# Kernel optimization log

Measured on AMD Instinct MI355X. Metric: run time of the kernel, lower is better.

The kernel has to match this reference:

```python
import jax, jax.numpy as jnp
import numpy as np

TEMP = 1.0  # routing_temperature

def _gelu(x):
    return jax.nn.gelu(x, approximate=False)  # torch nn.GELU default (erf)

def setup_inputs() -> dict:
    key = jax.random.key(0)
    ks = jax.random.split(key, 6)
    B, S, D, E, I = 8, 2048, 768, 8, 3072
    H = I // 2
    def xav(k, shape):
        fan_in, fan_out = shape[-2], shape[-1]
        lim = float(np.sqrt(6.0 / (fan_in + fan_out)))
        return jax.random.uniform(k, shape, jnp.float32, -lim, lim)
    return {
        "x":  jax.random.normal(ks[0], (B, S, D), jnp.float32),
        "Wr": xav(ks[1], (D, E)),
        "br": jnp.zeros((E,), jnp.float32),
        "W1": xav(ks[2], (E, D, I)), "b1": jnp.zeros((E, I), jnp.float32),
        "W2": xav(ks[3], (E, I, H)), "b2": jnp.zeros((E, H), jnp.float32),
        "W3": xav(ks[4], (E, H, D)), "b3": jnp.zeros((E, D), jnp.float32),
        "top_k": 2,
    }

def reference(x, Wr, br, W1, b1, W2, b2, W3, b3, top_k):
    B, S, D = x.shape
    E = Wr.shape[1]
    T = B * S
    xt = x.reshape(T, D)                              # flatten tokens
    logits = (xt @ Wr + br) / TEMP                    # [T, E]
    vals, sel = jax.lax.top_k(logits, top_k)          # [T, k]
    w = jax.nn.softmax(vals, axis=-1)                 # softmax over top-k scores
    # dense per-token combine weights (zero for unselected experts)
    combine = jnp.zeros((T, E), x.dtype).at[jnp.arange(T)[:, None], sel].add(w)
    def step(acc, p):
        W1e, b1e, W2e, b2e, W3e, b3e, ce = p
        h = _gelu(xt @ W1e + b1e)                     # [T, I]
        h = _gelu(h @ W2e + b2e)                      # [T, I//2]
        y = h @ W3e + b3e                             # [T, D]
        return acc + ce[:, None] * y, None
    acc0 = jnp.zeros((T, D), x.dtype)
    out, _ = jax.lax.scan(step, acc0, (W1, b1, W2, b2, W3, b3, combine.T))
    return out.reshape(B, S, D)
```

## Files before the change

kernel.cpp:

```cpp
#include <hip/hip_runtime.h>
#include <hip/hip_fp16.h>
#include <cstdint>
#include <cstddef>

#define TK 16384
#define DD 768
#define EE 8
#define II 3072
#define HH 1536

typedef _Float16 half8 __attribute__((ext_vector_type(8)));
typedef float floatx4 __attribute__((ext_vector_type(4)));

typedef const __attribute__((address_space(1))) uint32_t* gptr_t;
typedef __attribute__((address_space(3))) uint32_t* lptr_t;

#define GLOAD_LDS16(gp, lp) __builtin_amdgcn_global_load_lds( \
    (gptr_t)(const void*)(gp), (lptr_t)(void*)(lp), 16, 0, 0)

__device__ __forceinline__ void xcd_swizzle(int& e, int& m, int& n, bool rev) {
  int gx = gridDim.x, gy = gridDim.y;
  int f = (blockIdx.z * gy + blockIdx.y) * gx + blockIdx.x;
  if (rev) f = gx * gy * 8 - 1 - f;
  int xcd = f & 7, idx = f >> 3;
  int chunk = idx / gx, pos = idx - chunk * gx;
  int logical = chunk * (8 * gx) + xcd * gx + pos;
  int mn = gy * gx;
  e = logical / mn;
  int rem = logical - e * mn;
  m = rem / gx;
  n = rem - m * gx;
}

__global__ __launch_bounds__(256)
void cvtT_kernel(const float* __restrict__ in, __half* __restrict__ out,
                 int K, int N) {
  __shared__ float tile[64][65];
  int e = blockIdx.z;
  const float* inp = in + (size_t)e * K * N + (size_t)(blockIdx.y * 64) * N + blockIdx.x * 64;
  __half* outp = out + (size_t)e * K * N + (size_t)(blockIdx.x * 64) * K + blockIdx.y * 64;
  int s = threadIdx.x;
  int tx = s & 15, r0 = s >> 4;
#pragma unroll
  for (int i = 0; i < 4; ++i) {
    int k = r0 + i * 16;
    float4 v = *(const float4*)&inp[(size_t)k * N + tx * 4];
    tile[k][tx * 4 + 0] = v.x;
    tile[k][tx * 4 + 1] = v.y;
    tile[k][tx * 4 + 2] = v.z;
    tile[k][tx * 4 + 3] = v.w;
  }
  __syncthreads();
  int kp = s & 31;
#pragma unroll
  for (int i = 0; i < 8; ++i) {
    int n = (s >> 5) + i * 8;
    __half2 h = __floats2half2_rn(tile[2 * kp][n], tile[2 * kp + 1][n]);
    *(__half2*)&outp[(size_t)n * K + kp * 2] = h;
  }
}

__global__ __launch_bounds__(256)
void router_kernel(const float* __restrict__ x, const float* __restrict__ Wr,
                   const float* __restrict__ br, int* __restrict__ counts,
                   int* __restrict__ sel, float* __restrict__ wTok,
                   __half* __restrict__ xh) {
  __shared__ float wr_s[EE * DD];
  for (int i = threadIdx.x; i < EE * DD; i += 256) {
    int d = i >> 3, e = i & 7;
    wr_s[e * DD + d] = Wr[i];
  }
  __syncthreads();
  int wid = threadIdx.x >> 6, lane = threadIdx.x & 63;
  int t = blockIdx.x * 4 + wid;
  const float* xt = x + (size_t)t * DD;
  float acc[EE];
#pragma unroll
  for (int e = 0; e < EE; ++e) acc[e] = 0.f;
  for (int d = lane; d < DD; d += 64) {
    float xv = xt[d];
#pragma unroll
    for (int e = 0; e < EE; ++e) acc[e] += xv * wr_s[e * DD + d];
  }
#pragma unroll
  for (int off = 32; off > 0; off >>= 1)
#pragma unroll
    for (int e = 0; e < EE; ++e) acc[e] += __shfl_xor(acc[e], off);
  if (lane == 0) {
    float v[EE];
#pragma unroll
    for (int e = 0; e < EE; ++e) v[e] = acc[e] + br[e];
    int i0 = 0;
#pragma unroll
    for (int e = 1; e < EE; ++e) if (v[e] > v[i0]) i0 = e;
    int i1 = (i0 == 0) ? 1 : 0;
#pragma unroll
    for (int e = 0; e < EE; ++e) if (e != i0 && v[e] > v[i1] && e != i1) { if (v[e] > v[i1]) i1 = e; }
    float e1 = __expf(v[i1] - v[i0]);
    float s = 1.f / (1.f + e1);
    sel[2 * t] = i0; sel[2 * t + 1] = i1;
    wTok[2 * t] = s; wTok[2 * t + 1] = e1 * s;
    atomicAdd(&counts[i0], 1);
    atomicAdd(&counts[i1], 1);
  }
  const float4* xr = (const float4*)xt;
  uint2* xo = (uint2*)(xh + (size_t)t * DD);
#pragma unroll
  for (int j = 0; j < 3; ++j) {
    float4 v = xr[lane + j * 64];
    __half2 a = __floats2half2_rn(v.x, v.y);
    __half2 b = __floats2half2_rn(v.z, v.w);
    uint2 p;
    p.x = *(const unsigned int*)&a;
    p.y = *(const unsigned int*)&b;
    xo[lane + j * 64] = p;
  }
}

__global__ void offsets_kernel(const int* __restrict__ counts, int* __restrict__ offsets,
                               int* __restrict__ cursors) {
  if (threadIdx.x == 0) {
    int o = 0;
    for (int e = 0; e < EE; ++e) { offsets[e] = o; cursors[e] = o; o += counts[e]; }
  }
}

__global__ void scatter_kernel(const int* __restrict__ sel, int* __restrict__ cursors,
                               int* __restrict__ idxList, int* __restrict__ posTok) {
  int t = blockIdx.x * 256 + threadIdx.x;
  if (t < TK) {
#pragma unroll
    for (int k = 0; k < 2; ++k) {
      int e = sel[2 * t + k];
      int p = atomicAdd(&cursors[e], 1);
      idxList[p] = t;
      posTok[2 * t + k] = p;
    }
  }
}

template<int KD, int ND, bool GATHER, bool GELU, bool REV>
__device__ __forceinline__
void ffn_body_big(const __half* __restrict__ A, const __half* __restrict__ Wt,
                  const float* __restrict__ Bias, __half* __restrict__ Out,
                  const int* __restrict__ counts, const int* __restrict__ offsets,
                  const int* __restrict__ idxList) {
  constexpr int NT = KD / 32;
  int e, mblk, nblk;
  xcd_swizzle(e, mblk, nblk, REV);
  const int cnt = counts[e];
  const int m0 = mblk * 256;
  if (cnt == 0 || m0 >= cnt) return;
  const int off = offsets[e];
  const int n0 = nblk * 256;
  const __half* We = Wt + (size_t)e * KD * ND;
  const float* be = Bias + (size_t)e * ND;

  __shared__ __align__(16) __half AsF[5 * 256 * 32];
  __shared__ __align__(16) __half BsF[4 * 256 * 32];

  const int tid = threadIdx.x;
  const int colh = (((tid & 3) ^ ((tid >> 3) & 3)) << 3);
  const __half* aptr2[2];
  const __half* bptr2[2];
#pragma unroll
  for (int i = 0; i < 2; ++i) {
    int r = i * 128 + (tid >> 2);
    int gr = m0 + r; if (gr > cnt - 1) gr = cnt - 1;
    size_t arow = GATHER ? (size_t)idxList[off + gr] : (size_t)(off + gr);
    aptr2[i] = A + arow * KD + colh;
    bptr2[i] = We + (size_t)(n0 + r) * KD + colh;
  }

#define STA(WOFF, TS) do { \
    GLOAD_LDS16(aptr2[0] + (TS) * 32, (char*)AsF + (WOFF) + tid * 16); \
    GLOAD_LDS16(aptr2[1] + (TS) * 32, (char*)AsF + (WOFF) + tid * 16 + 8192); } while (0)
#define STB(WOFF, TS) do { \
    GLOAD_LDS16(bptr2[0] + (TS) * 32, (char*)BsF + (WOFF) + tid * 16); \
    GLOAD_LDS16(bptr2[1] + (TS) * 32, (char*)BsF + (WOFF) + tid * 16 + 8192); } while (0)

  const int lane = tid & 63, wv = tid >> 6;
  const int wr = wv >> 2, wc = wv & 3;
  const int lrow = lane & 15, lg = lane >> 4;
  const int slotSwz = lg ^ ((lrow >> 1) & 3);
  const int aBase = (wr * 128 + lrow) * 64 + slotSwz * 16;
  const int bBase = (wc * 64 + lrow) * 64 + slotSwz * 16;

  floatx4 acc[8][4];
#pragma unroll
  for (int mi = 0; mi < 8; ++mi)
#pragma unroll
    for (int ni = 0; ni < 4; ++ni) acc[mi][ni] = (floatx4){0.f, 0.f, 0.f, 0.f};

  STA(0 * 16384, 0);
  STB(0 * 16384, 0);
  STA(1 * 16384, 1);
  STB(1 * 16384, 1);
  STA(2 * 16384, 2);
  STB(2 * 16384, 2);
  STA(3 * 16384, 3);
  asm volatile("s_waitcnt vmcnt(10)" ::: "memory");
  __builtin_amdgcn_s_barrier();
  __builtin_amdgcn_sched_barrier(0);

  int rA = 0, wA = 4 * 16384;
  int rB = 0, wB = 3 * 16384;

#pragma unroll 1
  for (int t = 0; t < NT; ++t) {
    half8 af[8], bf[4];
#pragma unroll
    for (int mi = 0; mi < 8; ++mi)
      af[mi] = *(const half8*)((const char*)AsF + rA + aBase + mi * 1024);
#pragma unroll
    for (int ni = 0; ni < 4; ++ni)
      bf[ni] = *(const half8*)((const char*)BsF + rB + bBase + ni * 1024);
    if (t + 3 < NT) STB(wB, t + 3);
    if (t + 4 < NT) STA(wA, t + 4);
    __builtin_amdgcn_s_setprio(1);
#pragma unroll
    for (int mi = 0; mi < 8; ++mi)
#pragma unroll
      for (int ni = 0; ni < 4; ++ni)
        acc[mi][ni] = __builtin_amdgcn_mfma_f32_16x16x32_f16(
            af[mi], bf[ni], acc[mi][ni], 0, 0, 0);
    __builtin_amdgcn_s_setprio(0);
    if (t + 4 < NT) { asm volatile("s_waitcnt vmcnt(10)" ::: "memory"); }
    else            { asm volatile("s_waitcnt vmcnt(0)"  ::: "memory"); }
    __builtin_amdgcn_s_barrier();
    __builtin_amdgcn_sched_barrier(0);
    rA += 16384; if (rA == 5 * 16384) rA = 0;
    wA += 16384; if (wA == 5 * 16384) wA = 0;
    rB += 16384; if (rB == 4 * 16384) rB = 0;
    wB += 16384; if (wB == 4 * 16384) wB = 0;
  }

  const int crow = m0 + wr * 128 + lg * 4;
  const int ccol = n0 + wc * 64 + lrow;
  float bv[4];
#pragma unroll
  for (int ni = 0; ni < 4; ++ni) bv[ni] = be[ccol + ni * 16];
#pragma unroll
  for (int mi = 0; mi < 8; ++mi) {
#pragma unroll
    for (int j = 0; j < 4; ++j) {
      int r = crow + mi * 16 + j;
      if (r < cnt) {
#pragma unroll
        for (int ni = 0; ni < 4; ++ni) {
          float v = acc[mi][ni][j] + bv[ni];
          if (GELU) v = 0.5f * v * (1.f + erff(v * 0.70710678118654752f));
          Out[(size_t)(off + r) * ND + ccol + ni * 16] = __float2half(v);
        }
      }
    }
  }
#undef STA
#undef STB
}

template<int KD, int ND, bool GATHER, bool GELU, bool REV>
__device__ __forceinline__
void ffn_body_small(const __half* __restrict__ A, const __half* __restrict__ Wt,
                    const float* __restrict__ Bias, __half* __restrict__ Out,
                    const int* __restrict__ counts, const int* __restrict__ offsets,
                    const int* __restrict__ idxList) {
  constexpr int NT = KD / 32;
  int e, mblk, nblk;
  xcd_swizzle(e, mblk, nblk, REV);
  const int cnt = counts[e];
  const int m0 = mblk * 128;
  if (cnt == 0 || m0 >= cnt) return;
  const int off = offsets[e];
  const int n0 = nblk * 128;
  const __half* We = Wt + (size_t)e * KD * ND;
  const float* be = Bias + (size_t)e * ND;

  __shared__ __align__(16) __half AsF[3 * 128 * 32];
  __shared__ __align__(16) __half BsF[3 * 128 * 32];

  const int tid = threadIdx.x;
  const int colh = (((tid & 3) ^ ((tid >> 3) & 3)) << 3);
  const __half* aptr2[2];
  const __half* bptr2[2];
#pragma unroll
  for (int i = 0; i < 2; ++i) {
    int r = i * 64 + (tid >> 2);
    int gr = m0 + r; if (gr > cnt - 1) gr = cnt - 1;
    size_t arow = GATHER ? (size_t)idxList[off + gr] : (size_t)(off + gr);
    aptr2[i] = A + arow * KD + colh;
    bptr2[i] = We + (size_t)(n0 + r) * KD + colh;
  }

#define STA(WOFF, TS) do { \
    GLOAD_LDS16(aptr2[0] + (TS) * 32, (char*)AsF + (WOFF) + tid * 16); \
    GLOAD_LDS16(aptr2[1] + (TS) * 32, (char*)AsF + (WOFF) + tid * 16 + 4096); } while (0)
#define STB(WOFF, TS) do { \
    GLOAD_LDS16(bptr2[0] + (TS) * 32, (char*)BsF + (WOFF) + tid * 16); \
    GLOAD_LDS16(bptr2[1] + (TS) * 32, (char*)BsF + (WOFF) + tid * 16 + 4096); } while (0)

  const int lane = tid & 63, wv = tid >> 6;
  const int wr = wv >> 1, wc = wv & 1;
  const int lrow = lane & 15, lg = lane >> 4;
  const int slotSwz = lg ^ ((lrow >> 1) & 3);
  const int aBase = (wr * 64 + lrow) * 64 + slotSwz * 16;
  const int bBase = (wc * 64 + lrow) * 64 + slotSwz * 16;

  floatx4 acc[4][4];
#pragma unroll
  for (int mi = 0; mi < 4; ++mi)
#pragma unroll
    for (int ni = 0; ni < 4; ++ni) acc[mi][ni] = (floatx4){0.f, 0.f, 0.f, 0.f};

  STB(0, 0);
  STA(0, 0);
  STB(8192, 1);
  STA(8192, 1);
  asm volatile("s_waitcnt vmcnt(4)" ::: "memory");
  __builtin_amdgcn_s_barrier();
  __builtin_amdgcn_sched_barrier(0);

  int rBuf = 0, wBuf = 2 * 8192;

#pragma unroll 1
  for (int t = 0; t < NT; ++t) {
    half8 af[4], bf[4];
#pragma unroll
    for (int mi = 0; mi < 4; ++mi)
      af[mi] = *(const half8*)((const char*)AsF + rBuf + aBase + mi * 1024);
#pragma unroll
    for (int ni = 0; ni < 4; ++ni)
      bf[ni] = *(const half8*)((const char*)BsF + rBuf + bBase + ni * 1024);
    if (t + 2 < NT) { STB(wBuf, t + 2); STA(wBuf, t + 2); }
    __builtin_amdgcn_s_setprio(1);
#pragma unroll
    for (int mi = 0; mi < 4; ++mi)
#pragma unroll
      for (int ni = 0; ni < 4; ++ni)
        acc[mi][ni] = __builtin_amdgcn_mfma_f32_16x16x32_f16(
            af[mi], bf[ni], acc[mi][ni], 0, 0, 0);
    __builtin_amdgcn_s_setprio(0);
    if (t + 2 < NT) { asm volatile("s_waitcnt vmcnt(4)" ::: "memory"); }
    else            { asm volatile("s_waitcnt vmcnt(0)" ::: "memory"); }
    __builtin_amdgcn_s_barrier();
    __builtin_amdgcn_sched_barrier(0);
    rBuf += 8192; if (rBuf == 3 * 8192) rBuf = 0;
    wBuf += 8192; if (wBuf == 3 * 8192) wBuf = 0;
  }

  const int crow = m0 + wr * 64 + lg * 4;
  const int ccol = n0 + wc * 64 + lrow;
  float bv[4];
#pragma unroll
  for (int ni = 0; ni < 4; ++ni) bv[ni] = be[ccol + ni * 16];
#pragma unroll
  for (int mi = 0; mi < 4; ++mi) {
#pragma unroll
    for (int j = 0; j < 4; ++j) {
      int r = crow + mi * 16 + j;
      if (r < cnt) {
#pragma unroll
        for (int ni = 0; ni < 4; ++ni) {
          float v = acc[mi][ni][j] + bv[ni];
          if (GELU) v = 0.5f * v * (1.f + erff(v * 0.70710678118654752f));
          Out[(size_t)(off + r) * ND + ccol + ni * 16] = __float2half(v);
        }
      }
    }
  }
#undef STA
#undef STB
}

__global__ __launch_bounds__(256, 2)
void ffn_s1(const __half* __restrict__ A, const __half* __restrict__ Wt,
            const float* __restrict__ Bias, __half* __restrict__ Out,
            const int* __restrict__ counts, const int* __restrict__ offsets,
            const int* __restrict__ idxL) {
  ffn_body_small<DD, II, true, true, false>(A, Wt, Bias, Out, counts, offsets, idxL);
}
__global__ __launch_bounds__(512, 1)
void ffn_s2(const __half* __restrict__ A, const __half* __restrict__ Wt,
            const float* __restrict__ Bias, __half* __restrict__ Out,
            const int* __restrict__ counts, const int* __restrict__ offsets,
            const int* __restrict__ idxL) {
  ffn_body_big<II, HH, false, true, true>(A, Wt, Bias, Out, counts, offsets, idxL);
}
__global__ __launch_bounds__(256, 2)
void ffn_s3(const __half* __restrict__ A, const __half* __restrict__ Wt,
            const float* __restrict__ Bias, __half* __restrict__ Out,
            const int* __restrict__ counts, const int* __restrict__ offsets,
            const int* __restrict__ idxL) {
  ffn_body_small<HH, DD, false, false, false>(A, Wt, Bias, Out, counts, offsets, idxL);
}

__global__ void combine_kernel(const __half* __restrict__ yc, const float* __restrict__ wTok,
                               const int* __restrict__ posTok, float* __restrict__ out) {
  int t = blockIdx.x;
  int d = threadIdx.x * 4;
  if (d >= DD) return;
  float w0 = wTok[2 * t], w1 = wTok[2 * t + 1];
  const __half2* a = (const __half2*)(yc + (size_t)posTok[2 * t] * DD + d);
  const __half2* b = (const __half2*)(yc + (size_t)posTok[2 * t + 1] * DD + d);
  float2 a0 = __half22float2(a[0]), a1 = __half22float2(a[1]);
  float2 b0 = __half22float2(b[0]), b1 = __half22float2(b[1]);
  float4 r;
  r.x = w0 * a0.x + w1 * b0.x;
  r.y = w0 * a0.y + w1 * b0.y;
  r.z = w0 * a1.x + w1 * b1.x;
  r.w = w0 * a1.y + w1 * b1.y;
  *(float4*)(out + (size_t)t * DD + d) = r;
}

extern "C" void kernel_launch(void* const* d_in, const int* in_sizes, int n_in,
                              void* d_out, int out_size, void* d_ws, size_t ws_size,
                              hipStream_t stream) {
  const float* x  = (const float*)d_in[0];
  const float* Wr = (const float*)d_in[1];
  const float* br = (const float*)d_in[2];
  const float* W1 = (const float*)d_in[3];
  const float* b1 = (const float*)d_in[4];
  const float* W2 = (const float*)d_in[5];
  const float* b2 = (const float*)d_in[6];
  const float* W3 = (const float*)d_in[7];
  const float* b3 = (const float*)d_in[8];
  float* out = (float*)d_out;

  char* ws = (char*)d_ws;
  size_t o = 0;
  auto alloc = [&](size_t bytes) {
    char* p = ws + o;
    o += (bytes + 255) & ~(size_t)255;
    return p;
  };
  __half* xh   = (__half*)alloc((size_t)TK * DD * 2);
  __half* w1t  = (__half*)alloc((size_t)EE * DD * II * 2);
  __half* w2t  = (__half*)alloc((size_t)EE * II * HH * 2);
  __half* w3t  = (__half*)alloc((size_t)EE * HH * DD * 2);
  __half* h1   = (__half*)alloc((size_t)2 * TK * II * 2);
  __half* h2   = (__half*)alloc((size_t)2 * TK * HH * 2);
  __half* yc   = (__half*)alloc((size_t)2 * TK * DD * 2);
  int*   idxL  = (int*)alloc(2 * TK * 4);
  int*   sel   = (int*)alloc(2 * TK * 4);
  float* wTok  = (float*)alloc(2 * TK * 4);
  int*   posT  = (int*)alloc(2 * TK * 4);
  int*   counts  = (int*)alloc(256);
  int*   offsets = (int*)alloc(256);
  int*   cursors = (int*)alloc(256);
  if (o > ws_size) return;

  hipMemsetAsync(counts, 0, 256, stream);

  cvtT_kernel<<<dim3(II / 64, DD / 64, EE), 256, 0, stream>>>(W1, w1t, DD, II);
  cvtT_kernel<<<dim3(HH / 64, II / 64, EE), 256, 0, stream>>>(W2, w2t, II, HH);
  cvtT_kernel<<<dim3(DD / 64, HH / 64, EE), 256, 0, stream>>>(W3, w3t, HH, DD);
  router_kernel<<<TK / 4, 256, 0, stream>>>(x, Wr, br, counts, sel, wTok, xh);
  offsets_kernel<<<1, 64, 0, stream>>>(counts, offsets, cursors);
  scatter_kernel<<<TK / 256, 256, 0, stream>>>(sel, cursors, idxL, posT);

  ffn_s1<<<dim3(II / 128, 128, EE), 256, 0, stream>>>(xh, w1t, b1, h1, counts, offsets, idxL);
  ffn_s2<<<dim3(HH / 256, 64, EE), 512, 0, stream>>>(h1, w2t, b2, h2, counts, offsets, idxL);
  ffn_s3<<<dim3(DD / 128, 128, EE), 256, 0, stream>>>(h2, w3t, b3, yc, counts, offsets, idxL);

  combine_kernel<<<TK, 192, 0, stream>>>(yc, wTok, posT, out);
}
```

Before: 1.425 ms.

## Use BK=64 big-tile GEMM with 3/2-stage LDS ring for stages 1 and 2

Rewrites the 256x256 GEMM body to load 64-wide K slices per iteration, with a 3-buffer A and 2-buffer B ring instead of 5/4 buffers at K=32, and an 8-way XOR swizzle to match. Stage 1 now uses this big-tile kernel with 512 threads instead of the 128x128 small kernel, raising data reuse per block. The aim is to halve barriers per K and improve arithmetic intensity. In exchange, prefetch depth is shallower and stage 1 launches fewer, larger blocks, which may leave CUs underused.

```diff
diff --git a/kernel.cpp b/kernel.cpp
--- a/kernel.cpp
+++ b/kernel.cpp
@@ -141,11 +141,11 @@
 
 template<int KD, int ND, bool GATHER, bool GELU, bool REV>
 __device__ __forceinline__
-void ffn_body_big(const __half* __restrict__ A, const __half* __restrict__ Wt,
-                  const float* __restrict__ Bias, __half* __restrict__ Out,
-                  const int* __restrict__ counts, const int* __restrict__ offsets,
-                  const int* __restrict__ idxList) {
-  constexpr int NT = KD / 32;
+void ffn_body_big64(const __half* __restrict__ A, const __half* __restrict__ Wt,
+                    const float* __restrict__ Bias, __half* __restrict__ Out,
+                    const int* __restrict__ counts, const int* __restrict__ offsets,
+                    const int* __restrict__ idxList) {
+  constexpr int NT = KD / 64;
   int e, mblk, nblk;
   xcd_swizzle(e, mblk, nblk, REV);
   const int cnt = counts[e];
@@ -156,35 +156,44 @@
   const __half* We = Wt + (size_t)e * KD * ND;
   const float* be = Bias + (size_t)e * ND;
 
-  __shared__ __align__(16) __half AsF[5 * 256 * 32];
-  __shared__ __align__(16) __half BsF[4 * 256 * 32];
+  __shared__ __align__(16) __half AsF[3 * 256 * 64];
+  __shared__ __align__(16) __half BsF[2 * 256 * 64];
 
   const int tid = threadIdx.x;
-  const int colh = (((tid & 3) ^ ((tid >> 3) & 3)) << 3);
-  const __half* aptr2[2];
-  const __half* bptr2[2];
-#pragma unroll
-  for (int i = 0; i < 2; ++i) {
-    int r = i * 128 + (tid >> 2);
+  const int colh = (((tid & 7) ^ ((tid >> 3) & 7)) << 3);
+  const __half* aptr[4];
+  const __half* bptr[4];
+#pragma unroll
+  for (int i = 0; i < 4; ++i) {
+    int r = i * 64 + (tid >> 3);
     int gr = m0 + r; if (gr > cnt - 1) gr = cnt - 1;
     size_t arow = GATHER ? (size_t)idxList[off + gr] : (size_t)(off + gr);
-    aptr2[i] = A + arow * KD + colh;
-    bptr2[i] = We + (size_t)(n0 + r) * KD + colh;
-  }
-
-#define STA(WOFF, TS) do { \
-    GLOAD_LDS16(aptr2[0] + (TS) * 32, (char*)AsF + (WOFF) + tid * 16); \
-    GLOAD_LDS16(aptr2[1] + (TS) * 32, (char*)AsF + (WOFF) + tid * 16 + 8192); } while (0)
-#define STB(WOFF, TS) do { \
-    GLOAD_LDS16(bptr2[0] + (TS) * 32, (char*)BsF + (WOFF) + tid * 16); \
-    GLOAD_LDS16(bptr2[1] + (TS) * 32, (char*)BsF + (WOFF) + tid * 16 + 8192); } while (0)
+    aptr[i] = A + arow * KD + colh;
+    bptr[i] = We + (size_t)(n0 + r) * KD + colh;
+  }
+
+#define STA4(WOFFH, TS) do { \
+    GLOAD_LDS16(aptr[0] + (TS) * 64, &AsF[(WOFFH) + 0 * 4096 + tid * 8]); \
+    GLOAD_LDS16(aptr[1] + (TS) * 64, &AsF[(WOFFH) + 1 * 4096 + tid * 8]); \
+    GLOAD_LDS16(aptr[2] + (TS) * 64, &AsF[(WOFFH) + 2 * 4096 + tid * 8]); \
+    GLOAD_LDS16(aptr[3] + (TS) * 64, &AsF[(WOFFH) + 3 * 4096 + tid * 8]); } while (0)
+#define STB4(WOFFH, TS) do { \
+    GLOAD_LDS16(bptr[0] + (TS) * 64, &BsF[(WOFFH) + 0 * 4096 + tid * 8]); \
+    GLOAD_LDS16(bptr[1] + (TS) * 64, &BsF[(WOFFH) + 1 * 4096 + tid * 8]); \
+    GLOAD_LDS16(bptr[2] + (TS) * 64, &BsF[(WOFFH) + 2 * 4096 + tid * 8]); \
+    GLOAD_LDS16(bptr[3] + (TS) * 64, &BsF[(WOFFH) + 3 * 4096 + tid * 8]); } while (0)
 
   const int lane = tid & 63, wv = tid >> 6;
   const int wr = wv >> 2, wc = wv & 3;
   const int lrow = lane & 15, lg = lane >> 4;
-  const int slotSwz = lg ^ ((lrow >> 1) & 3);
-  const int aBase = (wr * 128 + lrow) * 64 + slotSwz * 16;
-  const int bBase = (wc * 64 + lrow) * 64 + slotSwz * 16;
+  int aoffh[2], boffh[2];
+#pragma unroll
+  for (int kk = 0; kk < 2; ++kk) {
+    int rowa = wr * 128 + lrow;
+    aoffh[kk] = rowa * 64 + (((kk * 4 + lg) ^ (rowa & 7)) << 3);
+    int rowb = wc * 64 + lrow;
+    boffh[kk] = rowb * 64 + (((kk * 4 + lg) ^ (rowb & 7)) << 3);
+  }
 
   floatx4 acc[8][4];
 #pragma unroll
@@ -192,47 +201,59 @@
 #pragma unroll
     for (int ni = 0; ni < 4; ++ni) acc[mi][ni] = (floatx4){0.f, 0.f, 0.f, 0.f};
 
-  STA(0 * 16384, 0);
-  STB(0 * 16384, 0);
-  STA(1 * 16384, 1);
-  STB(1 * 16384, 1);
-  STA(2 * 16384, 2);
-  STB(2 * 16384, 2);
-  STA(3 * 16384, 3);
-  asm volatile("s_waitcnt vmcnt(10)" ::: "memory");
+  STA4(0, 0);
+  STB4(0, 0);
+  STA4(16384, 1);
+  asm volatile("s_waitcnt vmcnt(4)" ::: "memory");
   __builtin_amdgcn_s_barrier();
   __builtin_amdgcn_sched_barrier(0);
 
-  int rA = 0, wA = 4 * 16384;
-  int rB = 0, wB = 3 * 16384;
+  int rA = 0, wA = 2 * 16384;
+  int rB = 0, wB = 16384;
 
 #pragma unroll 1
   for (int t = 0; t < NT; ++t) {
-    half8 af[8], bf[4];
-#pragma unroll
-    for (int mi = 0; mi < 8; ++mi)
-      af[mi] = *(const half8*)((const char*)AsF + rA + aBase + mi * 1024);
-#pragma unroll
-    for (int ni = 0; ni < 4; ++ni)
-      bf[ni] = *(const half8*)((const char*)BsF + rB + bBase + ni * 1024);
-    if (t + 3 < NT) STB(wB, t + 3);
-    if (t + 4 < NT) STA(wA, t + 4);
-    __builtin_amdgcn_s_setprio(1);
-#pragma unroll
-    for (int mi = 0; mi < 8; ++mi)
+    if (t + 1 < NT) STB4(wB, t + 1);
+    if (t + 2 < NT) STA4(wA, t + 2);
+    {
+      half8 af[8], bf[4];
+#pragma unroll
+      for (int mi = 0; mi < 8; ++mi)
+        af[mi] = *(const half8*)&AsF[rA + aoffh[0] + mi * 1024];
 #pragma unroll
       for (int ni = 0; ni < 4; ++ni)
-        acc[mi][ni] = __builtin_amdgcn_mfma_f32_16x16x32_f16(
-            af[mi], bf[ni], acc[mi][ni], 0, 0, 0);
-    __builtin_amdgcn_s_setprio(0);
-    if (t + 4 < NT) { asm volatile("s_waitcnt vmcnt(10)" ::: "memory"); }
-    else            { asm volatile("s_waitcnt vmcnt(0)"  ::: "memory"); }
+        bf[ni] = *(const half8*)&BsF[rB + boffh[0] + ni * 1024];
+      __builtin_amdgcn_s_setprio(1);
+#pragma unroll
+      for (int mi = 0; mi < 8; ++mi)
+#pragma unroll
+        for (int ni = 0; ni < 4; ++ni)
+          acc[mi][ni] = __builtin_amdgcn_mfma_f32_16x16x32_f16(
+              af[mi], bf[ni], acc[mi][ni], 0, 0, 0);
+      __builtin_amdgcn_s_setprio(0);
+#pragma unroll
+      for (int mi = 0; mi < 8; ++mi)
+        af[mi] = *(const half8*)&AsF[rA + aoffh[1] + mi * 1024];
+#pragma unroll
+      for (int ni = 0; ni < 4; ++ni)
+        bf[ni] = *(const half8*)&BsF[rB + boffh[1] + ni * 1024];
+      __builtin_amdgcn_s_setprio(1);
+#pragma unroll
+      for (int mi = 0; mi < 8; ++mi)
+#pragma unroll
+        for (int ni = 0; ni < 4; ++ni)
+          acc[mi][ni] = __builtin_amdgcn_mfma_f32_16x16x32_f16(
+              af[mi], bf[ni], acc[mi][ni], 0, 0, 0);
+      __builtin_amdgcn_s_setprio(0);
+    }
+    if (t + 2 < NT) { asm volatile("s_waitcnt vmcnt(4)" ::: "memory"); }
+    else            { asm volatile("s_waitcnt vmcnt(0)" ::: "memory"); }
     __builtin_amdgcn_s_barrier();
     __builtin_amdgcn_sched_barrier(0);
-    rA += 16384; if (rA == 5 * 16384) rA = 0;
-    wA += 16384; if (wA == 5 * 16384) wA = 0;
-    rB += 16384; if (rB == 4 * 16384) rB = 0;
-    wB += 16384; if (wB == 4 * 16384) wB = 0;
+    rA += 16384; if (rA == 3 * 16384) rA = 0;
+    wA += 16384; if (wA == 3 * 16384) wA = 0;
+    rB ^= 16384;
+    wB ^= 16384;
   }
 
   const int crow = m0 + wr * 128 + lg * 4;
@@ -255,8 +276,8 @@
       }
     }
   }
-#undef STA
-#undef STB
+#undef STA4
+#undef STB4
 }
 
 template<int KD, int ND, bool GATHER, bool GELU, bool REV>
@@ -372,19 +393,19 @@
 #undef STB
 }
 
-__global__ __launch_bounds__(256, 2)
+__global__ __launch_bounds__(512, 1)
 void ffn_s1(const __half* __restrict__ A, const __half* __restrict__ Wt,
             const float* __restrict__ Bias, __half* __restrict__ Out,
             const int* __restrict__ counts, const int* __restrict__ offsets,
             const int* __restrict__ idxL) {
-  ffn_body_small<DD, II, true, true, false>(A, Wt, Bias, Out, counts, offsets, idxL);
+  ffn_body_big64<DD, II, true, true, false>(A, Wt, Bias, Out, counts, offsets, idxL);
 }
 __global__ __launch_bounds__(512, 1)
 void ffn_s2(const __half* __restrict__ A, const __half* __restrict__ Wt,
             const float* __restrict__ Bias, __half* __restrict__ Out,
             const int* __restrict__ counts, const int* __restrict__ offsets,
             const int* __restrict__ idxL) {
-  ffn_body_big<II, HH, false, true, true>(A, Wt, Bias, Out, counts, offsets, idxL);
+  ffn_body_big64<II, HH, false, true, true>(A, Wt, Bias, Out, counts, offsets, idxL);
 }
 __global__ __launch_bounds__(256, 2)
 void ffn_s3(const __half* __restrict__ A, const __half* __restrict__ Wt,
@@ -458,7 +479,7 @@
   offsets_kernel<<<1, 64, 0, stream>>>(counts, offsets, cursors);
   scatter_kernel<<<TK / 256, 256, 0, stream>>>(sel, cursors, idxL, posT);
 
-  ffn_s1<<<dim3(II / 128, 128, EE), 256, 0, stream>>>(xh, w1t, b1, h1, counts, offsets, idxL);
+  ffn_s1<<<dim3(II / 256, 64, EE), 512, 0, stream>>>(xh, w1t, b1, h1, counts, offsets, idxL);
   ffn_s2<<<dim3(HH / 256, 64, EE), 512, 0, stream>>>(h1, w2t, b2, h2, counts, offsets, idxL);
   ffn_s3<<<dim3(DD / 128, 128, EE), 256, 0, stream>>>(h2, w3t, b3, yc, counts, offsets, idxL);
 
```

After: 1.539 ms. 8.0% more time.

## Fuse weighted combine into final expert GEMM epilogue via atomic adds

Applied to the files above, without the earlier changes.

The third expert GEMM now scales each output row by its routing weight and atomically adds it in fp32 straight into the zeroed output, using a per-slot weight array built by the scatter kernel. This removes the fp16 yc intermediate buffer and the separate combine kernel pass. In exchange it adds a memset of the output and scattered fp32 atomics, which can contend and make the summation order nondeterministic.

```diff
diff --git a/kernel.cpp b/kernel.cpp
--- a/kernel.cpp
+++ b/kernel.cpp
@@ -125,8 +125,9 @@
   }
 }
 
-__global__ void scatter_kernel(const int* __restrict__ sel, int* __restrict__ cursors,
-                               int* __restrict__ idxList, int* __restrict__ posTok) {
+__global__ void scatter_kernel(const int* __restrict__ sel, const float* __restrict__ wTok,
+                               int* __restrict__ cursors, int* __restrict__ idxList,
+                               float* __restrict__ wSlot) {
   int t = blockIdx.x * 256 + threadIdx.x;
   if (t < TK) {
 #pragma unroll
@@ -134,7 +135,7 @@
       int e = sel[2 * t + k];
       int p = atomicAdd(&cursors[e], 1);
       idxList[p] = t;
-      posTok[2 * t + k] = p;
+      wSlot[p] = wTok[2 * t + k];
     }
   }
 }
@@ -372,6 +373,120 @@
 #undef STB
 }
 
+template<int KD, int ND, bool REV>
+__device__ __forceinline__
+void ffn_body_small_fused(const __half* __restrict__ A, const __half* __restrict__ Wt,
+                          const float* __restrict__ Bias, float* __restrict__ Out,
+                          const int* __restrict__ counts, const int* __restrict__ offsets,
+                          const int* __restrict__ idxList, const float* __restrict__ wSlot) {
+  constexpr int NT = KD / 32;
+  int e, mblk, nblk;
+  xcd_swizzle(e, mblk, nblk, REV);
+  const int cnt = counts[e];
+  const int m0 = mblk * 128;
+  if (cnt == 0 || m0 >= cnt) return;
+  const int off = offsets[e];
+  const int n0 = nblk * 128;
+  const __half* We = Wt + (size_t)e * KD * ND;
+  const float* be = Bias + (size_t)e * ND;
+
+  __shared__ __align__(16) __half AsF[3 * 128 * 32];
+  __shared__ __align__(16) __half BsF[3 * 128 * 32];
+
+  const int tid = threadIdx.x;
+  const int colh = (((tid & 3) ^ ((tid >> 3) & 3)) << 3);
+  const __half* aptr2[2];
+  const __half* bptr2[2];
+#pragma unroll
+  for (int i = 0; i < 2; ++i) {
+    int r = i * 64 + (tid >> 2);
+    int gr = m0 + r; if (gr > cnt - 1) gr = cnt - 1;
+    size_t arow = (size_t)(off + gr);
+    aptr2[i] = A + arow * KD + colh;
+    bptr2[i] = We + (size_t)(n0 + r) * KD + colh;
+  }
+
+#define STA(WOFF, TS) do { \
+    GLOAD_LDS16(aptr2[0] + (TS) * 32, (char*)AsF + (WOFF) + tid * 16); \
+    GLOAD_LDS16(aptr2[1] + (TS) * 32, (char*)AsF + (WOFF) + tid * 16 + 4096); } while (0)
+#define STB(WOFF, TS) do { \
+    GLOAD_LDS16(bptr2[0] + (TS) * 32, (char*)BsF + (WOFF) + tid * 16); \
+    GLOAD_LDS16(bptr2[1] + (TS) * 32, (char*)BsF + (WOFF) + tid * 16 + 4096); } while (0)
+
+  const int lane = tid & 63, wv = tid >> 6;
+  const int wr = wv >> 1, wc = wv & 1;
+  const int lrow = lane & 15, lg = lane >> 4;
+  const int slotSwz = lg ^ ((lrow >> 1) & 3);
+  const int aBase = (wr * 64 + lrow) * 64 + slotSwz * 16;
+  const int bBase = (wc * 64 + lrow) * 64 + slotSwz * 16;
+
+  floatx4 acc[4][4];
+#pragma unroll
+  for (int mi = 0; mi < 4; ++mi)
+#pragma unroll
+    for (int ni = 0; ni < 4; ++ni) acc[mi][ni] = (floatx4){0.f, 0.f, 0.f, 0.f};
+
+  STB(0, 0);
+  STA(0, 0);
+  STB(8192, 1);
+  STA(8192, 1);
+  asm volatile("s_waitcnt vmcnt(4)" ::: "memory");
+  __builtin_amdgcn_s_barrier();
+  __builtin_amdgcn_sched_barrier(0);
+
+  int rBuf = 0, wBuf = 2 * 8192;
+
+#pragma unroll 1
+  for (int t = 0; t < NT; ++t) {
+    half8 af[4], bf[4];
+#pragma unroll
+    for (int mi = 0; mi < 4; ++mi)
+      af[mi] = *(const half8*)((const char*)AsF + rBuf + aBase + mi * 1024);
+#pragma unroll
+    for (int ni = 0; ni < 4; ++ni)
+      bf[ni] = *(const half8*)((const char*)BsF + rBuf + bBase + ni * 1024);
+    if (t + 2 < NT) { STB(wBuf, t + 2); STA(wBuf, t + 2); }
+    __builtin_amdgcn_s_setprio(1);
+#pragma unroll
+    for (int mi = 0; mi < 4; ++mi)
+#pragma unroll
+      for (int ni = 0; ni < 4; ++ni)
+        acc[mi][ni] = __builtin_amdgcn_mfma_f32_16x16x32_f16(
+            af[mi], bf[ni], acc[mi][ni], 0, 0, 0);
+    __builtin_amdgcn_s_setprio(0);
+    if (t + 2 < NT) { asm volatile("s_waitcnt vmcnt(4)" ::: "memory"); }
+    else            { asm volatile("s_waitcnt vmcnt(0)" ::: "memory"); }
+    __builtin_amdgcn_s_barrier();
+    __builtin_amdgcn_sched_barrier(0);
+    rBuf += 8192; if (rBuf == 3 * 8192) rBuf = 0;
+    wBuf += 8192; if (wBuf == 3 * 8192) wBuf = 0;
+  }
+
+  const int crow = m0 + wr * 64 + lg * 4;
+  const int ccol = n0 + wc * 64 + lrow;
+  float bv[4];
+#pragma unroll
+  for (int ni = 0; ni < 4; ++ni) bv[ni] = be[ccol + ni * 16];
+#pragma unroll
+  for (int mi = 0; mi < 4; ++mi) {
+#pragma unroll
+    for (int j = 0; j < 4; ++j) {
+      int r = crow + mi * 16 + j;
+      if (r < cnt) {
+        int slot = off + r;
+        int token = idxList[slot];
+        float w = wSlot[slot];
+        float* orow = Out + (size_t)token * ND + ccol;
+#pragma unroll
+        for (int ni = 0; ni < 4; ++ni)
+          atomicAdd(orow + ni * 16, w * (acc[mi][ni][j] + bv[ni]));
+      }
+    }
+  }
+#undef STA
+#undef STB
+}
+
 __global__ __launch_bounds__(256, 2)
 void ffn_s1(const __half* __restrict__ A, const __half* __restrict__ Wt,
             const float* __restrict__ Bias, __half* __restrict__ Out,
@@ -388,28 +503,10 @@
 }
 __global__ __launch_bounds__(256, 2)
 void ffn_s3(const __half* __restrict__ A, const __half* __restrict__ Wt,
-            const float* __restrict__ Bias, __half* __restrict__ Out,
+            const float* __restrict__ Bias, float* __restrict__ Out,
             const int* __restrict__ counts, const int* __restrict__ offsets,
-            const int* __restrict__ idxL) {
-  ffn_body_small<HH, DD, false, false, false>(A, Wt, Bias, Out, counts, offsets, idxL);
-}
-
-__global__ void combine_kernel(const __half* __restrict__ yc, const float* __restrict__ wTok,
-                               const int* __restrict__ posTok, float* __restrict__ out) {
-  int t = blockIdx.x;
-  int d = threadIdx.x * 4;
-  if (d >= DD) return;
-  float w0 = wTok[2 * t], w1 = wTok[2 * t + 1];
-  const __half2* a = (const __half2*)(yc + (size_t)posTok[2 * t] * DD + d);
-  const __half2* b = (const __half2*)(yc + (size_t)posTok[2 * t + 1] * DD + d);
-  float2 a0 = __half22float2(a[0]), a1 = __half22float2(a[1]);
-  float2 b0 = __half22float2(b[0]), b1 = __half22float2(b[1]);
-  float4 r;
-  r.x = w0 * a0.x + w1 * b0.x;
-  r.y = w0 * a0.y + w1 * b0.y;
-  r.z = w0 * a1.x + w1 * b1.x;
-  r.w = w0 * a1.y + w1 * b1.y;
-  *(float4*)(out + (size_t)t * DD + d) = r;
+            const int* __restrict__ idxL, const float* __restrict__ wSlot) {
+  ffn_body_small_fused<HH, DD, false>(A, Wt, Bias, Out, counts, offsets, idxL, wSlot);
 }
 
 extern "C" void kernel_launch(void* const* d_in, const int* in_sizes, int n_in,
@@ -439,28 +536,26 @@
   __half* w3t  = (__half*)alloc((size_t)EE * HH * DD * 2);
   __half* h1   = (__half*)alloc((size_t)2 * TK * II * 2);
   __half* h2   = (__half*)alloc((size_t)2 * TK * HH * 2);
-  __half* yc   = (__half*)alloc((size_t)2 * TK * DD * 2);
   int*   idxL  = (int*)alloc(2 * TK * 4);
   int*   sel   = (int*)alloc(2 * TK * 4);
   float* wTok  = (float*)alloc(2 * TK * 4);
-  int*   posT  = (int*)alloc(2 * TK * 4);
+  float* wSlot = (float*)alloc(2 * TK * 4);
   int*   counts  = (int*)alloc(256);
   int*   offsets = (int*)alloc(256);
   int*   cursors = (int*)alloc(256);
   if (o > ws_size) return;
 
   hipMemsetAsync(counts, 0, 256, stream);
+  hipMemsetAsync(out, 0, (size_t)out_size * sizeof(float), stream);
 
   cvtT_kernel<<<dim3(II / 64, DD / 64, EE), 256, 0, stream>>>(W1, w1t, DD, II);
   cvtT_kernel<<<dim3(HH / 64, II / 64, EE), 256, 0, stream>>>(W2, w2t, II, HH);
   cvtT_kernel<<<dim3(DD / 64, HH / 64, EE), 256, 0, stream>>>(W3, w3t, HH, DD);
   router_kernel<<<TK / 4, 256, 0, stream>>>(x, Wr, br, counts, sel, wTok, xh);
   offsets_kernel<<<1, 64, 0, stream>>>(counts, offsets, cursors);
-  scatter_kernel<<<TK / 256, 256, 0, stream>>>(sel, cursors, idxL, posT);
+  scatter_kernel<<<TK / 256, 256, 0, stream>>>(sel, wTok, cursors, idxL, wSlot);
 
   ffn_s1<<<dim3(II / 128, 128, EE), 256, 0, stream>>>(xh, w1t, b1, h1, counts, offsets, idxL);
   ffn_s2<<<dim3(HH / 256, 64, EE), 512, 0, stream>>>(h1, w2t, b2, h2, counts, offsets, idxL);
-  ffn_s3<<<dim3(DD / 128, 128, EE), 256, 0, stream>>>(h2, w3t, b3, yc, counts, offsets, idxL);
-
-  combine_kernel<<<TK, 192, 0, stream>>>(yc, wTok, posT, out);
-}
+  ffn_s3<<<dim3(DD / 128, 128, EE), 256, 0, stream>>>(h2, w3t, b3, out, counts, offsets, idxL, wSlot);
+}
```

New measurement: 1.470 ms. 1.03x slower.
